# Optimization experiments

Hardware: AMD Instinct MI355X
Metric: run time of the kernel (lower is better)

## Reference

```python
import jax, jax.numpy as jnp
import numpy as np

NEG_SLOPE = 0.01  # torch LeakyReLU default


def setup_inputs() -> dict:
    N, H, Da, A, E, T, M = 100000, 256, 128, 250000, 60000, 512, 20000
    key = jax.random.key(0)
    ks = jax.random.split(key, 10)
    inp = {
        "nodes_representations": jax.random.normal(ks[0], (N, H), dtype=jnp.float32),
        "hyperedge_arg_node_idxs": jax.random.randint(ks[1], (A,), 0, N),
        "unq_hyperedge_type_reprs": jax.random.normal(ks[2], (T, H), dtype=jnp.float32),
        "hyperedge_type_name_unq_idxs": jax.random.randint(ks[3], (E,), 0, T),
        "unq_hyperedge_arg_name_reprs": jax.random.normal(ks[4], (M, Da), dtype=jnp.float32),
        "hyperedge_arg_name_unq_idxs": jax.random.randint(ks[5], (A,), 0, M),
        "hyperedge_arg_to_edge_id": jax.random.randint(ks[6], (A,), 0, E),
        "num_edges": E,
        "W1": jax.random.normal(ks[7], (H + Da, H), dtype=jnp.float32) * 0.05,
        "b1": jnp.zeros((H,), dtype=jnp.float32),
        "W2": jax.random.normal(ks[8], (2 * H + Da, H), dtype=jnp.float32) * 0.05,
        "b2": jnp.zeros((H,), dtype=jnp.float32),
    }
    return inp


def reference(nodes_representations, hyperedge_arg_node_idxs, unq_hyperedge_type_reprs,
              hyperedge_type_name_unq_idxs, unq_hyperedge_arg_name_reprs,
              hyperedge_arg_name_unq_idxs, hyperedge_arg_to_edge_id, num_edges,
              W1, b1, W2, b2):
    # Gather per-arg name and node reprs, concat -> [A, Da+H]
    arg_name = unq_hyperedge_arg_name_reprs[hyperedge_arg_name_unq_idxs]
    arg_node = nodes_representations[hyperedge_arg_node_idxs]
    arg_reprs = jnp.concatenate([arg_name, arg_node], axis=-1)

    Da = arg_name.shape[1]
    # Edge type reprs [E, H], zero-padded to [E, H+Da] (branch always taken here)
    edge_type = unq_hyperedge_type_reprs[hyperedge_type_name_unq_idxs]
    edge_type = jnp.concatenate(
        [edge_type, jnp.zeros((edge_type.shape[0], Da), dtype=edge_type.dtype)], axis=-1)

    # Message MLP on stacked [A+E, H+Da]
    all_in = jnp.concatenate([arg_reprs, edge_type], axis=0)
    msgs = jax.nn.leaky_relu(all_in @ W1 + b1, negative_slope=NEG_SLOPE)

    # Segment-max grouped by edge id (every edge gets its own type message, so no empty segments)
    seg_ids = jnp.concatenate(
        [hyperedge_arg_to_edge_id, jnp.arange(num_edges, dtype=hyperedge_arg_to_edge_id.dtype)])
    edge_states = jax.ops.segment_max(msgs, seg_ids, num_segments=num_edges)

    # Update MLP: gather edge state per arg, concat with arg reprs -> [A, 2H+Da]
    # (Dropout is identity in eval mode.)
    upd_in = jnp.concatenate([edge_states[hyperedge_arg_to_edge_id], arg_reprs], axis=1)
    message_to_nodes = jax.nn.leaky_relu(upd_in @ W2 + b2, negative_slope=NEG_SLOPE)
    return (message_to_nodes, edge_states)
```

## Files before the change

kernel.cpp:

```cpp
#include <hip/hip_runtime.h>
#include <stdint.h>

#define A_CNT 250000
#define E_CNT 60000
#define N_NODES 100000
#define M_NAMES 20000
#define T_TYPES 512
#define H_DIM 256
#define DA    128
#define K1    384
#define K2    640
#define NEG_SLOPE 0.01f
#define SENT  0xFFFFFFFFu
#define LDSZ  (128 * 32)

typedef float v4f __attribute__((ext_vector_type(4)));
typedef short v8s __attribute__((ext_vector_type(8)));
typedef unsigned short u16;

__device__ __forceinline__ unsigned enc_f(float f) {
    unsigned u = __float_as_uint(f);
    return (u & 0x80000000u) ? ~u : (u | 0x80000000u);
}
__device__ __forceinline__ float dec_f(unsigned e) {
    unsigned u = (e & 0x80000000u) ? (e & 0x7FFFFFFFu) : ~e;
    return __uint_as_float(u);
}
__device__ __forceinline__ u16 f2bf(float f) {
    unsigned u = __float_as_uint(f);
    u += 0x7FFFu + ((u >> 16) & 1u);
    return (u16)(u >> 16);
}
__device__ __forceinline__ uint4 pack8(float4 a, float4 b) {
    union { u16 u[8]; uint4 v; } p;
    p.u[0]=f2bf(a.x); p.u[1]=f2bf(a.y); p.u[2]=f2bf(a.z); p.u[3]=f2bf(a.w);
    p.u[4]=f2bf(b.x); p.u[5]=f2bf(b.y); p.u[6]=f2bf(b.z); p.u[7]=f2bf(b.w);
    return p.v;
}

__device__ __forceinline__ void gload16(const u16* g, u16* l) {
    __builtin_amdgcn_global_load_lds(
        (const __attribute__((address_space(1))) unsigned int*)(g),
        (__attribute__((address_space(3))) unsigned int*)(l), 16, 0, 0);
}

__global__ void wprep_kernel(const float* __restrict__ W, u16* __restrict__ Wt, int K) {
    int k = blockIdx.x, c = threadIdx.x;
    Wt[(size_t)c * K + k] = f2bf(W[(size_t)k * 256 + c]);
}

__global__ void tobf16_kernel(const float* __restrict__ in, u16* __restrict__ out, int n8) {
    int i = blockIdx.x * 256 + threadIdx.x;
    if (i < n8) {
        const float4* p = (const float4*)in + (size_t)2 * i;
        float4 a = p[0], b = p[1];
        ((uint4*)out)[i] = pack8(a, b);
    }
}

__global__ void hist_kernel(const int* __restrict__ arg_edge, unsigned* __restrict__ counts) {
    int i = blockIdx.x * 256 + threadIdx.x;
    if (i < A_CNT) atomicAdd(&counts[arg_edge[i]], 1u);
}

__global__ __launch_bounds__(1024) void scan_kernel(const unsigned* __restrict__ counts,
                                                    unsigned* __restrict__ cursor) {
    __shared__ unsigned sd[1024];
    const int tid = threadIdx.x;
    const int CH = (E_CNT + 1023) / 1024;
    const int base = tid * CH;
    unsigned s = 0;
    for (int i = 0; i < CH; ++i) { int idx = base + i; if (idx < E_CNT) s += counts[idx]; }
    sd[tid] = s; __syncthreads();
    for (int d = 1; d < 1024; d <<= 1) {
        unsigned v = (tid >= d) ? sd[tid - d] : 0u; __syncthreads();
        sd[tid] += v; __syncthreads();
    }
    unsigned run = sd[tid] - s;
    for (int i = 0; i < CH; ++i) {
        int idx = base + i;
        if (idx < E_CNT) { cursor[idx] = run; run += counts[idx]; }
    }
}

__global__ void scatter_kernel(const int* __restrict__ arg_edge, unsigned* __restrict__ cursor,
                               unsigned* __restrict__ perm, unsigned* __restrict__ sorted_edge) {
    int i = blockIdx.x * 256 + threadIdx.x;
    if (i < A_CNT) {
        int e = arg_edge[i];
        unsigned pos = atomicAdd(&cursor[e], 1u);
        perm[pos] = (unsigned)i;
        sorted_edge[pos] = (unsigned)e;
    }
}

__global__ __launch_bounds__(256, 3) void gemm1_kernel(
    const u16* __restrict__ nodes_bf, const int* __restrict__ arg_node_idx,
    const u16* __restrict__ types_bf, const int* __restrict__ type_idx,
    const u16* __restrict__ names_bf, const int* __restrict__ arg_name_idx,
    const unsigned* __restrict__ perm, const unsigned* __restrict__ sorted_edge,
    const u16* __restrict__ Wt1, const float* __restrict__ b1,
    const u16* __restrict__ zbuf,
    unsigned* __restrict__ enc)
{
    __shared__ __align__(16) u16 sX[2 * LDSZ];
    __shared__ __align__(16) u16 sW[2 * LDSZ];
    const int t = threadIdx.x;
    const int lane = t & 63, wave = t >> 6;
    const int row0 = blockIdx.x * 128;
    const int col0 = blockIdx.y * 128;

    const int rsub = wave * 16 + (lane >> 2);
    const int slot = lane & 3;

    const u16* xs0[2]; const u16* xs1[2]; int xcls[2];
    const u16* ws[2];
    u16* xdst[2]; u16* wdst[2];
    #pragma unroll
    for (int c = 0; c < 2; ++c) {
        const int rloc = c * 64 + rsub;
        const int ss = slot ^ ((rloc >> 1) & 3);
        const int gr = row0 + rloc;
        if (gr < A_CNT) {
            int aid = (int)perm[gr];
            xcls[c] = 0;
            xs0[c] = names_bf + (size_t)arg_name_idx[aid] * DA + ss * 8;
            xs1[c] = nodes_bf + (size_t)arg_node_idx[aid] * H_DIM + ss * 8 - DA;
        } else if (gr < A_CNT + E_CNT) {
            xcls[c] = 1;
            xs0[c] = types_bf + (size_t)type_idx[gr - A_CNT] * H_DIM + ss * 8;
            xs1[c] = zbuf;
        } else {
            xcls[c] = 2; xs0[c] = zbuf; xs1[c] = zbuf;
        }
        ws[c]   = Wt1 + (size_t)(col0 + rloc) * K1 + ss * 8;
        xdst[c] = &sX[(c * 64 + wave * 16) * 32];
        wdst[c] = &sW[(c * 64 + wave * 16) * 32];
    }

    const int wr = (wave & 1) * 64, wc = (wave >> 1) * 64;
    const int lm = lane & 15, lq = lane >> 4;

    int xoff[4], woff[4];
    #pragma unroll
    for (int i = 0; i < 4; ++i) {
        int ra = wr + i * 16 + lm;
        xoff[i] = ra * 32 + (lq ^ ((ra >> 1) & 3)) * 8;
        int rb = wc + i * 16 + lm;
        woff[i] = rb * 32 + (lq ^ ((rb >> 1) & 3)) * 8;
    }

    v4f acc[4][4];
    #pragma unroll
    for (int i = 0; i < 4; ++i)
        #pragma unroll
        for (int j = 0; j < 4; ++j) acc[i][j] = (v4f)0.f;

    auto stage = [&](int buf, int kc) {
        #pragma unroll
        for (int c = 0; c < 2; ++c) {
            const u16* xsrc;
            if (xcls[c] == 0)      xsrc = ((kc < DA) ? xs0[c] : xs1[c]) + kc;
            else if (xcls[c] == 1) xsrc = (kc < H_DIM) ? (xs0[c] + kc) : zbuf;
            else                   xsrc = zbuf;
            gload16(xsrc, xdst[c] + buf * LDSZ);
            gload16(ws[c] + kc, wdst[c] + buf * LDSZ);
        }
    };

    const int nt = K1 / 32;
    stage(0, 0);
    for (int tt = 0; tt < nt; ++tt) {
        if (tt + 1 < nt) {
            stage((tt + 1) & 1, (tt + 1) * 32);
            asm volatile("s_waitcnt vmcnt(4)" ::: "memory");
        } else {
            asm volatile("s_waitcnt vmcnt(0)" ::: "memory");
        }
        __builtin_amdgcn_sched_barrier(0);
        __builtin_amdgcn_s_barrier();
        __builtin_amdgcn_sched_barrier(0);

        const u16* bx = &sX[(tt & 1) * LDSZ];
        const u16* bw = &sW[(tt & 1) * LDSZ];
        v8s af[4], bf[4];
        #pragma unroll
        for (int i = 0; i < 4; ++i) af[i] = *(const v8s*)&bx[xoff[i]];
        #pragma unroll
        for (int j = 0; j < 4; ++j) bf[j] = *(const v8s*)&bw[woff[j]];
        #pragma unroll
        for (int i = 0; i < 4; ++i)
            #pragma unroll
            for (int j = 0; j < 4; ++j)
                acc[i][j] = __builtin_amdgcn_mfma_f32_16x16x32_bf16(af[i], bf[j], acc[i][j], 0, 0, 0);

        __builtin_amdgcn_sched_barrier(0);
        __builtin_amdgcn_s_barrier();
    }

    float bb[4];
    #pragma unroll
    for (int j = 0; j < 4; ++j) bb[j] = b1[col0 + wc + j*16 + lm];

    #pragma unroll
    for (int i = 0; i < 4; ++i) {
        const int r0 = row0 + wr + i*16 + lq*4;
        unsigned seg[4];
        #pragma unroll
        for (int reg = 0; reg < 4; ++reg) {
            int g = r0 + reg;
            seg[reg] = (g < A_CNT) ? sorted_edge[g]
                     : (g < A_CNT + E_CNT ? (unsigned)(g - A_CNT) : SENT);
        }
        #pragma unroll
        for (int j = 0; j < 4; ++j) {
            const int cj = col0 + wc + j*16 + lm;
            float v[4];
            #pragma unroll
            for (int reg = 0; reg < 4; ++reg) {
                float y = acc[i][j][reg] + bb[j];
                v[reg] = (y >= 0.f) ? y : NEG_SLOPE * y;
            }
            unsigned cs = seg[0]; float m = v[0];
            #pragma unroll
            for (int reg = 1; reg < 4; ++reg) {
                if (seg[reg] == cs) { m = fmaxf(m, v[reg]); }
                else {
                    if (cs != SENT) atomicMax(&enc[(size_t)cs * H_DIM + cj], enc_f(m));
                    cs = seg[reg]; m = v[reg];
                }
            }
            if (cs != SENT) atomicMax(&enc[(size_t)cs * H_DIM + cj], enc_f(m));
        }
    }
}

__global__ void decode_kernel(unsigned* __restrict__ enc, u16* __restrict__ es_bf) {
    size_t i = (size_t)blockIdx.x * 1024 + threadIdx.x;
    const size_t n4 = (size_t)E_CNT * H_DIM / 4;
    if (i < n4) {
        uint4 e = ((const uint4*)enc)[i];
        float4 f;
        f.x = dec_f(e.x); f.y = dec_f(e.y); f.z = dec_f(e.z); f.w = dec_f(e.w);
        ((float4*)enc)[i] = f;
        union { u16 u[4]; unsigned long long v; } p;
        p.u[0]=f2bf(f.x); p.u[1]=f2bf(f.y); p.u[2]=f2bf(f.z); p.u[3]=f2bf(f.w);
        ((unsigned long long*)es_bf)[i] = p.v;
    }
}

__global__ __launch_bounds__(256, 3) void gemm2_kernel(
    const u16* __restrict__ nodes_bf, const int* __restrict__ arg_node_idx,
    const u16* __restrict__ names_bf, const int* __restrict__ arg_name_idx,
    const int* __restrict__ arg_edge, const u16* __restrict__ es_bf,
    const u16* __restrict__ Wt2, const float* __restrict__ b2,
    const u16* __restrict__ zbuf,
    float* __restrict__ out)
{
    __shared__ __align__(16) u16 sX[2 * LDSZ];
    __shared__ __align__(16) u16 sW[2 * LDSZ];
    const int t = threadIdx.x;
    const int lane = t & 63, wave = t >> 6;
    const int row0 = blockIdx.x * 128;
    const int col0 = blockIdx.y * 128;

    const int rsub = wave * 16 + (lane >> 2);
    const int slot = lane & 3;

    const u16* pe[2]; const u16* pn[2]; const u16* pd[2]; int valid[2];
    const u16* ws[2];
    u16* xdst[2]; u16* wdst[2];
    #pragma unroll
    for (int c = 0; c < 2; ++c) {
        const int rloc = c * 64 + rsub;
        const int ss = slot ^ ((rloc >> 1) & 3);
        const int gr = row0 + rloc;
        if (gr < A_CNT) {
            valid[c] = 1;
            pe[c] = es_bf   + (size_t)arg_edge[gr]      * H_DIM + ss * 8;
            pn[c] = names_bf + (size_t)arg_name_idx[gr] * DA    + ss * 8 - H_DIM;
            pd[c] = nodes_bf + (size_t)arg_node_idx[gr] * H_DIM + ss * 8 - H_DIM - DA;
        } else {
            valid[c] = 0; pe[c] = zbuf; pn[c] = zbuf; pd[c] = zbuf;
        }
        ws[c]   = Wt2 + (size_t)(col0 + rloc) * K2 + ss * 8;
        xdst[c] = &sX[(c * 64 + wave * 16) * 32];
        wdst[c] = &sW[(c * 64 + wave * 16) * 32];
    }

    const int wr = (wave & 1) * 64, wc = (wave >> 1) * 64;
    const int lm = lane & 15, lq = lane >> 4;

    int xoff[4], woff[4];
    #pragma unroll
    for (int i = 0; i < 4; ++i) {
        int ra = wr + i * 16 + lm;
        xoff[i] = ra * 32 + (lq ^ ((ra >> 1) & 3)) * 8;
        int rb = wc + i * 16 + lm;
        woff[i] = rb * 32 + (lq ^ ((rb >> 1) & 3)) * 8;
    }

    v4f acc[4][4];
    #pragma unroll
    for (int i = 0; i < 4; ++i)
        #pragma unroll
        for (int j = 0; j < 4; ++j) acc[i][j] = (v4f)0.f;

    auto stage = [&](int buf, int kc) {
        #pragma unroll
        for (int c = 0; c < 2; ++c) {
            const u16* xsrc;
            if (valid[c]) {
                const u16* p = (kc < H_DIM) ? pe[c] : ((kc < H_DIM + DA) ? pn[c] : pd[c]);
                xsrc = p + kc;
            } else xsrc = zbuf;
            gload16(xsrc, xdst[c] + buf * LDSZ);
            gload16(ws[c] + kc, wdst[c] + buf * LDSZ);
        }
    };

    const int nt = K2 / 32;
    stage(0, 0);
    for (int tt = 0; tt < nt; ++tt) {
        if (tt + 1 < nt) {
            stage((tt + 1) & 1, (tt + 1) * 32);
            asm volatile("s_waitcnt vmcnt(4)" ::: "memory");
        } else {
            asm volatile("s_waitcnt vmcnt(0)" ::: "memory");
        }
        __builtin_amdgcn_sched_barrier(0);
        __builtin_amdgcn_s_barrier();
        __builtin_amdgcn_sched_barrier(0);

        const u16* bx = &sX[(tt & 1) * LDSZ];
        const u16* bw = &sW[(tt & 1) * LDSZ];
        v8s af[4], bf[4];
        #pragma unroll
        for (int i = 0; i < 4; ++i) af[i] = *(const v8s*)&bx[xoff[i]];
        #pragma unroll
        for (int j = 0; j < 4; ++j) bf[j] = *(const v8s*)&bw[woff[j]];
        #pragma unroll
        for (int i = 0; i < 4; ++i)
            #pragma unroll
            for (int j = 0; j < 4; ++j)
                acc[i][j] = __builtin_amdgcn_mfma_f32_16x16x32_bf16(af[i], bf[j], acc[i][j], 0, 0, 0);

        __builtin_amdgcn_sched_barrier(0);
        __builtin_amdgcn_s_barrier();
    }

    float bb[4];
    #pragma unroll
    for (int j = 0; j < 4; ++j) bb[j] = b2[col0 + wc + j*16 + lm];

    #pragma unroll
    for (int i = 0; i < 4; ++i) {
        const int r0 = row0 + wr + i*16 + lq*4;
        #pragma unroll
        for (int reg = 0; reg < 4; ++reg) {
            const int g = r0 + reg;
            if (g < A_CNT) {
                #pragma unroll
                for (int j = 0; j < 4; ++j) {
                    float y = acc[i][j][reg] + bb[j];
                    y = (y >= 0.f) ? y : NEG_SLOPE * y;
                    out[(size_t)g * H_DIM + col0 + wc + j*16 + lm] = y;
                }
            }
        }
    }
}

extern "C" void kernel_launch(void* const* d_in, const int* in_sizes, int n_in,
                              void* d_out, int out_size, void* d_ws, size_t ws_size,
                              hipStream_t stream) {
    const float* nodes        = (const float*)d_in[0];
    const int*   arg_node_idx = (const int*)  d_in[1];
    const float* types        = (const float*)d_in[2];
    const int*   type_idx     = (const int*)  d_in[3];
    const float* names        = (const float*)d_in[4];
    const int*   arg_name_idx = (const int*)  d_in[5];
    const int*   arg_edge     = (const int*)  d_in[6];
    const float* W1           = (const float*)d_in[8];
    const float* b1           = (const float*)d_in[9];
    const float* W2           = (const float*)d_in[10];
    const float* b2           = (const float*)d_in[11];

    float* out_msg = (float*)d_out;
    float* out_es  = out_msg + (size_t)A_CNT * H_DIM;
    unsigned* enc  = (unsigned*)out_es;

    char* ws = (char*)d_ws;
    size_t off = 0;
    auto alloc = [&](size_t bytes) -> void* {
        void* p = ws + off;
        off = (off + bytes + 255) & ~(size_t)255;
        return p;
    };
    u16* Wt1          = (u16*)alloc((size_t)256 * K1 * sizeof(u16));
    u16* Wt2          = (u16*)alloc((size_t)256 * K2 * sizeof(u16));
    u16* es_bf        = (u16*)alloc((size_t)E_CNT * H_DIM * sizeof(u16));
    u16* nodes_bf     = (u16*)alloc((size_t)N_NODES * H_DIM * sizeof(u16));
    u16* names_bf     = (u16*)alloc((size_t)M_NAMES * DA * sizeof(u16));
    u16* types_bf     = (u16*)alloc((size_t)T_TYPES * H_DIM * sizeof(u16));
    u16* zbuf         = (u16*)alloc(256);
    unsigned* counts  = (unsigned*)alloc((size_t)E_CNT * sizeof(unsigned));
    unsigned* cursor  = (unsigned*)alloc((size_t)E_CNT * sizeof(unsigned));
    unsigned* perm    = (unsigned*)alloc((size_t)A_CNT * sizeof(unsigned));
    unsigned* sorted_edge = (unsigned*)alloc((size_t)A_CNT * sizeof(unsigned));

    hipMemsetAsync(counts, 0, (size_t)E_CNT * sizeof(unsigned), stream);
    hipMemsetAsync(enc, 0, (size_t)E_CNT * H_DIM * sizeof(unsigned), stream);
    hipMemsetAsync(zbuf, 0, 256, stream);

    wprep_kernel<<<K1, 256, 0, stream>>>(W1, Wt1, K1);
    wprep_kernel<<<K2, 256, 0, stream>>>(W2, Wt2, K2);
    {
        int n8 = N_NODES * H_DIM / 8;
        tobf16_kernel<<<(n8 + 255) / 256, 256, 0, stream>>>(nodes, nodes_bf, n8);
    }
    {
        int n8 = M_NAMES * DA / 8;
        tobf16_kernel<<<(n8 + 255) / 256, 256, 0, stream>>>(names, names_bf, n8);
    }
    {
        int n8 = T_TYPES * H_DIM / 8;
        tobf16_kernel<<<(n8 + 255) / 256, 256, 0, stream>>>(types, types_bf, n8);
    }
    hist_kernel<<<(A_CNT + 255) / 256, 256, 0, stream>>>(arg_edge, counts);
    scan_kernel<<<1, 1024, 0, stream>>>(counts, cursor);
    scatter_kernel<<<(A_CNT + 255) / 256, 256, 0, stream>>>(arg_edge, cursor, perm, sorted_edge);

    dim3 g1((A_CNT + E_CNT + 127) / 128, 2);
    gemm1_kernel<<<g1, 256, 0, stream>>>(nodes_bf, arg_node_idx, types_bf, type_idx,
                                         names_bf, arg_name_idx, perm, sorted_edge,
                                         Wt1, b1, zbuf, enc);
    decode_kernel<<<((E_CNT * H_DIM / 4) + 1023) / 1024, 1024, 0, stream>>>(enc, es_bf);

    dim3 g2((A_CNT + 127) / 128, 2);
    gemm2_kernel<<<g2, 256, 0, stream>>>(nodes_bf, arg_node_idx, names_bf, arg_name_idx,
                                         arg_edge, es_bf, Wt2, b2, zbuf, out_msg);
}
```

Baseline: 876.3 us.

## Precompute type messages per unique type and seed segment-max buffer

The edge-type rows of the first GEMM depend only on the 512 unique types, so the change computes the MLP output once per type in a small kernel. It then initialises the segment-max buffer by gathering those per-type messages, which replaces the zero memset. The first GEMM now covers only the argument rows. This removes about 60k redundant GEMM rows and their atomics. The trade-off is two extra small launches and a scalar dot-product kernel for the types.

```diff
diff --git a/kernel.cpp b/kernel.cpp
--- a/kernel.cpp
+++ b/kernel.cpp
@@ -94,9 +94,41 @@
     }
 }
 
+__global__ void tmsg_kernel(const u16* __restrict__ types_bf, const u16* __restrict__ Wt1,
+                            const float* __restrict__ b1, unsigned* __restrict__ tmsg_enc) {
+    const int tt = blockIdx.x, c = threadIdx.x;
+    const u16* xr = types_bf + (size_t)tt * H_DIM;
+    const u16* wr = Wt1 + (size_t)c * K1;
+    float acc = 0.f;
+    for (int k = 0; k < H_DIM; k += 8) {
+        v8s x = *(const v8s*)&xr[k];
+        v8s w = *(const v8s*)&wr[k];
+        #pragma unroll
+        for (int u = 0; u < 8; ++u) {
+            float xf = __uint_as_float((unsigned)(u16)x[u] << 16);
+            float wf = __uint_as_float((unsigned)(u16)w[u] << 16);
+            acc += xf * wf;
+        }
+    }
+    float y = acc + b1[c];
+    y = (y >= 0.f) ? y : NEG_SLOPE * y;
+    tmsg_enc[(size_t)tt * H_DIM + c] = enc_f(y);
+}
+
+__global__ void einit_kernel(const int* __restrict__ type_idx,
+                             const unsigned* __restrict__ tmsg_enc,
+                             unsigned* __restrict__ enc) {
+    size_t i = (size_t)blockIdx.x * 256 + threadIdx.x;
+    if (i < (size_t)E_CNT * (H_DIM / 4)) {
+        int e  = (int)(i >> 6);
+        int c4 = (int)(i & 63);
+        int tt = type_idx[e];
+        ((uint4*)enc)[i] = ((const uint4*)tmsg_enc)[(size_t)tt * 64 + c4];
+    }
+}
+
 __global__ __launch_bounds__(256, 3) void gemm1_kernel(
     const u16* __restrict__ nodes_bf, const int* __restrict__ arg_node_idx,
-    const u16* __restrict__ types_bf, const int* __restrict__ type_idx,
     const u16* __restrict__ names_bf, const int* __restrict__ arg_name_idx,
     const unsigned* __restrict__ perm, const unsigned* __restrict__ sorted_edge,
     const u16* __restrict__ Wt1, const float* __restrict__ b1,
@@ -113,7 +145,7 @@
     const int rsub = wave * 16 + (lane >> 2);
     const int slot = lane & 3;
 
-    const u16* xs0[2]; const u16* xs1[2]; int xcls[2];
+    const u16* xs0[2]; const u16* xs1[2]; int valid[2];
     const u16* ws[2];
     u16* xdst[2]; u16* wdst[2];
     #pragma unroll
@@ -123,15 +155,11 @@
         const int gr = row0 + rloc;
         if (gr < A_CNT) {
             int aid = (int)perm[gr];
-            xcls[c] = 0;
+            valid[c] = 1;
             xs0[c] = names_bf + (size_t)arg_name_idx[aid] * DA + ss * 8;
             xs1[c] = nodes_bf + (size_t)arg_node_idx[aid] * H_DIM + ss * 8 - DA;
-        } else if (gr < A_CNT + E_CNT) {
-            xcls[c] = 1;
-            xs0[c] = types_bf + (size_t)type_idx[gr - A_CNT] * H_DIM + ss * 8;
-            xs1[c] = zbuf;
         } else {
-            xcls[c] = 2; xs0[c] = zbuf; xs1[c] = zbuf;
+            valid[c] = 0; xs0[c] = zbuf; xs1[c] = zbuf;
         }
         ws[c]   = Wt1 + (size_t)(col0 + rloc) * K1 + ss * 8;
         xdst[c] = &sX[(c * 64 + wave * 16) * 32];
@@ -159,10 +187,7 @@
     auto stage = [&](int buf, int kc) {
         #pragma unroll
         for (int c = 0; c < 2; ++c) {
-            const u16* xsrc;
-            if (xcls[c] == 0)      xsrc = ((kc < DA) ? xs0[c] : xs1[c]) + kc;
-            else if (xcls[c] == 1) xsrc = (kc < H_DIM) ? (xs0[c] + kc) : zbuf;
-            else                   xsrc = zbuf;
+            const u16* xsrc = valid[c] ? (((kc < DA) ? xs0[c] : xs1[c]) + kc) : zbuf;
             gload16(xsrc, xdst[c] + buf * LDSZ);
             gload16(ws[c] + kc, wdst[c] + buf * LDSZ);
         }
@@ -209,8 +234,7 @@
         #pragma unroll
         for (int reg = 0; reg < 4; ++reg) {
             int g = r0 + reg;
-            seg[reg] = (g < A_CNT) ? sorted_edge[g]
-                     : (g < A_CNT + E_CNT ? (unsigned)(g - A_CNT) : SENT);
+            seg[reg] = (g < A_CNT) ? sorted_edge[g] : SENT;
         }
         #pragma unroll
         for (int j = 0; j < 4; ++j) {
@@ -403,6 +427,7 @@
     u16* nodes_bf     = (u16*)alloc((size_t)N_NODES * H_DIM * sizeof(u16));
     u16* names_bf     = (u16*)alloc((size_t)M_NAMES * DA * sizeof(u16));
     u16* types_bf     = (u16*)alloc((size_t)T_TYPES * H_DIM * sizeof(u16));
+    unsigned* tmsg_enc = (unsigned*)alloc((size_t)T_TYPES * H_DIM * sizeof(unsigned));
     u16* zbuf         = (u16*)alloc(256);
     unsigned* counts  = (unsigned*)alloc((size_t)E_CNT * sizeof(unsigned));
     unsigned* cursor  = (unsigned*)alloc((size_t)E_CNT * sizeof(unsigned));
@@ -410,7 +435,6 @@
     unsigned* sorted_edge = (unsigned*)alloc((size_t)A_CNT * sizeof(unsigned));
 
     hipMemsetAsync(counts, 0, (size_t)E_CNT * sizeof(unsigned), stream);
-    hipMemsetAsync(enc, 0, (size_t)E_CNT * H_DIM * sizeof(unsigned), stream);
     hipMemsetAsync(zbuf, 0, 256, stream);
 
     wprep_kernel<<<K1, 256, 0, stream>>>(W1, Wt1, K1);
@@ -431,8 +455,14 @@
     scan_kernel<<<1, 1024, 0, stream>>>(counts, cursor);
     scatter_kernel<<<(A_CNT + 255) / 256, 256, 0, stream>>>(arg_edge, cursor, perm, sorted_edge);
 
-    dim3 g1((A_CNT + E_CNT + 127) / 128, 2);
-    gemm1_kernel<<<g1, 256, 0, stream>>>(nodes_bf, arg_node_idx, types_bf, type_idx,
+    tmsg_kernel<<<T_TYPES, 256, 0, stream>>>(types_bf, Wt1, b1, tmsg_enc);
+    {
+        size_t n4 = (size_t)E_CNT * (H_DIM / 4);
+        einit_kernel<<<(unsigned)((n4 + 255) / 256), 256, 0, stream>>>(type_idx, tmsg_enc, enc);
+    }
+
+    dim3 g1((A_CNT + 127) / 128, 2);
+    gemm1_kernel<<<g1, 256, 0, stream>>>(nodes_bf, arg_node_idx,
                                          names_bf, arg_name_idx, perm, sorted_edge,
                                          Wt1, b1, zbuf, enc);
     decode_kernel<<<((E_CNT * H_DIM / 4) + 1023) / 1024, 1024, 0, stream>>>(enc, es_bf);
```

New measurement: 842.6 us. 3.8% less time.
